# Kernel tuning notes

Hardware: AMD Instinct MI355X
Metric: run time of the kernel (lower is better)

Reference implementation:

```python
import jax, jax.numpy as jnp
import numpy as np

# Fixed architecture constants from Cifar10Model / RetNetConfig
NL = 8            # num_layers
H = 4             # num_heads
D = 64            # hidden_size
QK = 64           # qk_dim
V = 128           # v_dim
QH, VH = QK // H, V // H   # 16, 32 per-head dims
P, IMG, C = 8, 32, 3       # patch size, image size, channels
NP = (IMG // P) ** 2       # 16 patches
T = NP + 1                 # +1 cls token -> 17 tokens
FFN = 12                   # ffn_proj_size


def layer_norm(x, s, b, eps=1e-5):
    mu = x.mean(-1, keepdims=True)
    var = x.var(-1, keepdims=True)
    return (x - mu) * jax.lax.rsqrt(var + eps) * s + b


def rotate_every_two(x):
    x1, x2 = x[..., ::2], x[..., 1::2]
    return jnp.stack([-x2, x1], axis=-1).reshape(x.shape)


def rel_pos(t):
    # xPos-style rotation angles over the per-head qk dim
    angle = 1.0 / (10000 ** jnp.linspace(0.0, 1.0, QH // 2))
    angle = jnp.repeat(angle, 2)                      # (QH,)
    idx = jnp.arange(t, dtype=jnp.float32)[:, None]
    sin, cos = jnp.sin(idx * angle), jnp.cos(idx * angle)   # (t, QH)
    # per-head retention decay gamma (use_default_gamma=False path)
    gamma = 1.0 - jnp.exp(jnp.linspace(np.log(1 / 32), np.log(1 / 512), H))  # (H,)
    n = jnp.arange(t)
    expo = n[:, None] - n[None, :]                    # n - m
    causal = expo >= 0
    dmask = jnp.where(causal, gamma[:, None, None] ** jnp.where(causal, expo, 0), 0.0)  # (H,t,t)
    dmask = dmask / jnp.sqrt(dmask.sum(-1, keepdims=True))   # row-normalized decay
    return sin, cos, dmask


def retention(x, Wq, Wk, Wv, Wg, Wo, sin, cos, dmask):
    b, t, _ = x.shape
    q = (x @ Wq).reshape(b, t, H, QH).transpose(0, 2, 1, 3)   # (b,h,t,qh)
    k = (x @ Wk).reshape(b, t, H, QH).transpose(0, 2, 1, 3)
    v = (x @ Wv).reshape(b, t, H, VH).transpose(0, 2, 1, 3)   # (b,h,t,vh)
    g = x @ Wg                                                # (b,t,V) gate
    q = q * cos + rotate_every_two(q) * sin
    k = (k * cos + rotate_every_two(k) * sin) * (QH ** -0.5)
    scores = jnp.einsum('bhnd,bhmd->bhnm', q, k) * dmask      # decay-masked QK^T
    denom = jnp.clip(jnp.abs(jax.lax.stop_gradient(scores).sum(-1, keepdims=True)), 1.0, None)
    scores = scores / denom                                   # retention row normalization
    o = jnp.einsum('bhnm,bhmd->bhnd', scores, v)              # (b,h,t,vh)
    # per-head group norm (no affine) instead of softmax normalization
    mu = o.mean(-1, keepdims=True)
    var = o.var(-1, keepdims=True)
    o = (o - mu) * jax.lax.rsqrt(var + 1e-5)
    o = o.transpose(0, 2, 1, 3).reshape(b, t, V)
    return (jax.nn.silu(g) * o) @ Wo


def setup_inputs() -> dict:
    key = jax.random.key(0)
    ks = iter(jax.random.split(key, 32))
    s = 0.02
    B = 8192
    inp = {
        'x': jax.random.normal(next(ks), (B, C, IMG, IMG), jnp.float32),
        'patch_w': jax.random.normal(next(ks), (C * P * P, D), jnp.float32) * s,
        'patch_b': jnp.zeros((D,), jnp.float32),
        'cls': jax.random.normal(next(ks), (1, 1, D), jnp.float32) * s,
        'pos': jax.random.normal(next(ks), (T, D), jnp.float32) * s,
        'Wq': jax.random.normal(next(ks), (NL, D, QK), jnp.float32) * s,
        'Wk': jax.random.normal(next(ks), (NL, D, QK), jnp.float32) * s,
        'Wv': jax.random.normal(next(ks), (NL, D, V), jnp.float32) * s,
        'Wg': jax.random.normal(next(ks), (NL, D, V), jnp.float32) * s,
        'Wo': jax.random.normal(next(ks), (NL, V, D), jnp.float32) * s,
        'ln1_s': jnp.ones((NL, D), jnp.float32),
        'ln1_b': jnp.zeros((NL, D), jnp.float32),
        'w1': jax.random.normal(next(ks), (NL, D, FFN), jnp.float32) * s,
        'b1': jnp.zeros((NL, FFN), jnp.float32),
        'w2': jax.random.normal(next(ks), (NL, FFN, D), jnp.float32) * s,
        'b2': jnp.zeros((NL, D), jnp.float32),
        'ln2_s': jnp.ones((NL, D), jnp.float32),
        'ln2_b': jnp.zeros((NL, D), jnp.float32),
        'lnf_s': jnp.ones((D,), jnp.float32),
        'lnf_b': jnp.zeros((D,), jnp.float32),
        'neck_w': jax.random.normal(next(ks), (D, 16), jnp.float32) * s,
        'neck_b': jnp.zeros((16,), jnp.float32),
        'head_w': jax.random.normal(next(ks), (16, 10), jnp.float32) * s,
        'head_b': jnp.zeros((10,), jnp.float32),
    }
    return inp


def reference(x, patch_w, patch_b, cls, pos, Wq, Wk, Wv, Wg, Wo, ln1_s, ln1_b,
              w1, b1, w2, b2, ln2_s, ln2_b, lnf_s, lnf_b, neck_w, neck_b, head_w, head_b):
    b = x.shape[0]
    # patch embedding: stride==kernel conv expressed as reshape + matmul
    xp = x.reshape(b, C, IMG // P, P, IMG // P, P).transpose(0, 2, 4, 1, 3, 5)
    xp = xp.reshape(b, NP, C * P * P)
    tok = xp @ patch_w + patch_b                          # (b,16,64)
    tok = jnp.concatenate([jnp.broadcast_to(cls, (b, 1, D)), tok], axis=1) + pos  # (b,17,64)
    sin, cos, dmask = rel_pos(T)
    h = tok
    for i in range(NL):  # pre-LN RetNet blocks
        h = h + retention(layer_norm(h, ln1_s[i], ln1_b[i]),
                          Wq[i], Wk[i], Wv[i], Wg[i], Wo[i], sin, cos, dmask)
        f = layer_norm(h, ln2_s[i], ln2_b[i])
        h = h + jax.nn.gelu(f @ w1[i] + b1[i]) @ w2[i] + b2[i]
    h = layer_norm(h, lnf_s, lnf_b)
    ys = h[:, -1, :]                                      # last token
    return (ys @ neck_w + neck_b) @ head_w + head_b       # (b,10) logits
```

## Files before the change

### kernel.cpp

```cpp
#include <hip/hip_runtime.h>
#include <hip/hip_bf16.h>

#define NLAY 8
#define MFMA __builtin_amdgcn_mfma_f32_16x16x32_bf16
#define MFMA32 __builtin_amdgcn_mfma_f32_32x32x16_bf16

typedef __attribute__((ext_vector_type(8))) short bf16x8;
typedef __attribute__((ext_vector_type(4))) float f32x4;
typedef __attribute__((ext_vector_type(16))) float f32x16;
typedef __attribute__((ext_vector_type(4))) int i32x4;

template <bool BF16>
__device__ __forceinline__ float ld(const void* p, int i) {
  if (BF16) {
    unsigned short u = ((const unsigned short*)p)[i];
    return __uint_as_float(((unsigned)u) << 16);
  }
  return ((const float*)p)[i];
}

template <bool BF16>
__device__ __forceinline__ float2 ld2(const void* p, int i) {
  float2 r;
  if (BF16) {
    unsigned u = ((const unsigned*)p)[i >> 1];
    r.x = __uint_as_float(u << 16);
    r.y = __uint_as_float(u & 0xffff0000u);
  } else {
    r = ((const float2*)p)[i >> 1];
  }
  return r;
}

__device__ __forceinline__ unsigned pack_bf2(float a, float b) {
  __hip_bfloat16 ha = __float2bfloat16(a), hb = __float2bfloat16(b);
  unsigned short ua, ub;
  __builtin_memcpy(&ua, &ha, 2);
  __builtin_memcpy(&ub, &hb, 2);
  return ((unsigned)ub << 16) | (unsigned)ua;
}

__device__ __forceinline__ unsigned short cvt_bf(float a) {
  __hip_bfloat16 h = __float2bfloat16(a);
  unsigned short us;
  __builtin_memcpy(&us, &h, 2);
  return us;
}

__device__ __forceinline__ float2 unpk(unsigned u) {
  float2 r;
  r.x = __uint_as_float(u << 16);
  r.y = __uint_as_float(u & 0xffff0000u);
  return r;
}

__device__ __forceinline__ bf16x8 as_bf(i32x4 v) {
  bf16x8 r;
  __builtin_memcpy(&r, &v, 16);
  return r;
}

__global__ void setup_tables(float* __restrict__ ws, const void* __restrict__ x) {
  int tid = threadIdx.x;
  for (int idx = tid; idx < 272; idx += 256) {
    int t = idx >> 4, j = idx & 15;
    float a = powf(10000.f, -(float)(j >> 1) / 7.f);
    float arg = (float)t * a;
    ws[idx] = sinf(arg);
    ws[272 + idx] = cosf(arg);
  }
  for (int row = tid; row < 68; row += 256) {
    int hh = row / 17, t = row % 17;
    float gamma = 1.f - exp2f(-5.f - 4.f * (float)hh / 3.f);
    float sum = 0.f;
    for (int u = 0; u <= t; ++u) sum += powf(gamma, (float)(t - u));
    float rn = rsqrtf(sum);
    for (int u = 0; u < 17; ++u)
      ws[544 + row * 17 + u] = (u <= t) ? powf(gamma, (float)(t - u)) * rn : 0.f;
  }
  if (tid == 0) {
    const unsigned short* u16 = (const unsigned short*)x;
    int sane = 0;
    for (int i = 0; i < 128; ++i) {
      float v = __uint_as_float(((unsigned)u16[2 * i]) << 16);
      float av = fabsf(v);
      if (v == 0.f || (av > 1e-8f && av < 1e4f)) sane++;
    }
    ws[1700] = (sane >= 64) ? 1.f : 0.f;
  }
}

#define FRAG_OLD 280576
#define FRAG_TOT 305152
template <bool BF16>
__global__ void prep_frags(const void* __restrict__ patch_w,
                           const void* __restrict__ Wq, const void* __restrict__ Wk,
                           const void* __restrict__ Wv, const void* __restrict__ Wg,
                           const void* __restrict__ Wo, const void* __restrict__ w1,
                           const void* __restrict__ w2,
                           const float* __restrict__ tab,
                           unsigned short* __restrict__ frag) {
  if ((tab[1700] > 0.5f) != BF16) return;
  int g = blockIdx.x * 256 + threadIdx.x;
  if (g >= FRAG_TOT) return;
  float v;
  if (g < 12288) {
    int nt = g / 3072, r = g % 3072, kt = r / 512, r2 = r % 512, la = r2 >> 3, j = r2 & 7;
    int n = nt * 16 + (la & 15), k = kt * 32 + (la >> 4) * 8 + j;
    v = ld<BF16>(patch_w, k * 64 + n);
  } else if (g < FRAG_OLD) {
    int gg = g - 12288, l = gg / 33536, o = gg % 33536;
    if (o < 8192) {
      const void* W = (o < 4096) ? Wq : Wk;
      int e = o & 4095;
      int nt = e / 1024, r = e % 1024, kt = r / 512, r2 = r % 512, la = r2 >> 3, j = r2 & 7;
      int n = nt * 16 + (la & 15), k = kt * 32 + (la >> 4) * 8 + j;
      v = ld<BF16>(W, l * 4096 + k * 64 + n);
    } else if (o < 24576) {
      const void* W = (o < 16384) ? Wv : Wg;
      int e = (o - 8192) & 8191;
      int nt = e / 1024, r = e % 1024, kt = r / 512, r2 = r % 512, la = r2 >> 3, j = r2 & 7;
      int n = nt * 16 + (la & 15), k = kt * 32 + (la >> 4) * 8 + j;
      v = ld<BF16>(W, l * 8192 + k * 128 + n);
    } else if (o < 32768) {
      int e = o - 24576;
      int nt = e / 2048, r = e % 2048, kt = r / 512, r2 = r % 512, la = r2 >> 3, j = r2 & 7;
      int n = nt * 16 + (la & 15), k = kt * 32 + (la >> 4) * 8 + j;
      v = ld<BF16>(Wo, l * 8192 + k * 64 + n);
    } else {
      int e = o - 32768, eo = e / 64, d = e % 64;
      v = ld<BF16>(w1, l * 768 + d * 12 + eo);
    }
  } else {
    int gg = g - FRAG_OLD, l = gg / 3072, o = gg % 3072;
    if (o < 1024) {
      int kt = o >> 9, r = o & 511, la = r >> 3, j = r & 7;
      int n = la & 15, k = kt * 32 + (la >> 4) * 8 + j;
      v = (n < 12) ? ld<BF16>(w1, l * 768 + k * 12 + n) : 0.f;
    } else {
      int e2 = o - 1024;
      int nt = e2 >> 9, r = e2 & 511, la = r >> 3, j = r & 7;
      int n = nt * 16 + (la & 15), k = (la >> 4) * 8 + j;
      v = (k < 12) ? ld<BF16>(w2, (l * 12 + k) * 64 + n) : 0.f;
    }
  }
  __hip_bfloat16 h = __float2bfloat16(v);
  unsigned short us;
  __builtin_memcpy(&us, &h, 2);
  frag[g] = us;
}

#define O_DM   0
#define O_SIN  1156
#define O_COS  1428
#define O_ST   1700
#define O_H    2212
#define O_XNF  4456
#define O_FF   5992
#define O_R    6400
#define O_SCA  11024
#define O_VG   14096
#define SM_TOT 18968

template <bool BF16>
__global__ void __launch_bounds__(512, 4)
vit_fused(const void* __restrict__ x, const void* __restrict__ patch_b,
          const void* __restrict__ cls, const void* __restrict__ pos,
          const void* __restrict__ ln1s, const void* __restrict__ ln1b,
          const void* __restrict__ b1, const void* __restrict__ b2,
          const void* __restrict__ ln2s, const void* __restrict__ ln2b,
          const void* __restrict__ lnfs, const void* __restrict__ lnfb,
          const void* __restrict__ neckw, const void* __restrict__ neckb,
          const void* __restrict__ headw, const void* __restrict__ headb,
          const float* __restrict__ tab, const unsigned short* __restrict__ FR,
          void* __restrict__ out) {
  if ((tab[1700] > 0.5f) != BF16) return;

  const int tid = threadIdx.x;
  const int lane = tid & 63, w = tid >> 6;
  const int lq = lane >> 4, ln = lane & 15;
  const int img0 = 2 * blockIdx.x;

  __shared__ __align__(16) float sm[SM_TOT];
  float* sDM  = sm + O_DM;
  float* sSin = sm + O_SIN;
  float* sCos = sm + O_COS;
  float* sST  = sm + O_ST;
  float* sH   = sm + O_H;
  float* sFF  = sm + O_FF;
  float* sQ   = sm + O_R;
  float* sK   = sm + O_R + 2312;
  float* sO   = sm + O_R;
  unsigned short* sVbT = (unsigned short*)(sm + O_VG);
  unsigned short* sGb  = (unsigned short*)(sm + O_VG) + 5120;
  const bf16x8* FRB = (const bf16x8*)FR;

  for (int i = tid; i < 1156; i += 512) sDM[i] = tab[544 + i] * 0.25f;
  for (int i = tid; i < 272; i += 512) { sSin[i] = tab[i]; sCos[i] = tab[272 + i]; }
  for (int s = tid; s < 768; s += 512) {
    int mt = s / 384, r = s % 384, kt = r / 64, la = r % 64;
    int p = la & 15, q = la >> 4;
    int kb = kt * 32 + q * 8;
    int c = kb >> 6, rem = kb & 63, a = rem >> 3;
    int pi = p >> 2, pj = p & 3;
    int src = (img0 + mt) * 3072 + c * 1024 + (pi * 8 + a) * 32 + pj * 8;
    float v[8];
#pragma unroll
    for (int t2 = 0; t2 < 8; t2 += 2) {
      float2 pv = ld2<BF16>(x, src + t2);
      v[t2] = pv.x; v[t2 + 1] = pv.y;
    }
    i32x4 pk;
    pk.x = pack_bf2(v[0], v[1]); pk.y = pack_bf2(v[2], v[3]);
    pk.z = pack_bf2(v[4], v[5]); pk.w = pack_bf2(v[6], v[7]);
    ((i32x4*)(sm + O_SCA))[s] = pk;
  }
  if (tid < 128) {
    int img = tid >> 6, n = tid & 63;
    sH[(img * 17) * 66 + n] = ld<BF16>(cls, n) + ld<BF16>(pos, n);
  }
  __syncthreads();

  {
    int mt = w >> 2, nt = w & 3;
    f32x4 acc = {0.f, 0.f, 0.f, 0.f};
    const bf16x8* paf = (const bf16x8*)(sm + O_SCA);
#pragma unroll
    for (int kt = 0; kt < 6; ++kt)
      acc = MFMA(paf[(mt * 6 + kt) * 64 + lane], FRB[(nt * 6 + kt) * 64 + lane], acc, 0, 0, 0);
    int n = nt * 16 + ln;
    float pb = ld<BF16>(patch_b, n);
#pragma unroll
    for (int i = 0; i < 4; ++i) {
      int t = 1 + lq * 4 + i;
      sH[(mt * 17 + t) * 66 + n] = acc[i] + pb + ld<BF16>(pos, t * 64 + n);
    }
  }
  __syncthreads();

  for (int l = 0; l < NLAY; ++l) {
    const int LB = 1536 + l * 4192;

    if (tid < 320) {
      int la = tid & 63, wv = tid >> 6;
      int m = wv * 8 + (la & 7);
      int sub = ((la >> 3) & 3) + 4 * (la >> 5);
      i32x4 pk = {0, 0, 0, 0};
      if (m < 34) {
        const float2* hp = (const float2*)(sH + m * 66 + sub * 8);
        float2 h0 = hp[0], h1 = hp[1], h2 = hp[2], h3 = hp[3];
        float s1 = 0.f, s2 = 0.f;
        s1 += h0.x; s2 += h0.x * h0.x; s1 += h0.y; s2 += h0.y * h0.y;
        s1 += h1.x; s2 += h1.x * h1.x; s1 += h1.y; s2 += h1.y * h1.y;
        s1 += h2.x; s2 += h2.x * h2.x; s1 += h2.y; s2 += h2.y * h2.y;
        s1 += h3.x; s2 += h3.x * h3.x; s1 += h3.y; s2 += h3.y * h3.y;
        s1 += __shfl_xor(s1, 8);  s2 += __shfl_xor(s2, 8);
        s1 += __shfl_xor(s1, 16); s2 += __shfl_xor(s2, 16);
        s1 += __shfl_xor(s1, 32); s2 += __shfl_xor(s2, 32);
        float mu = s1 * (1.f / 64.f);
        float var = s2 * (1.f / 64.f) - mu * mu;
        float rr = rsqrtf(var + 1e-5f);
        int kb = sub * 8;
        float hv[8] = {h0.x, h0.y, h1.x, h1.y, h2.x, h2.y, h3.x, h3.y};
        float vv[8];
#pragma unroll
        for (int t2 = 0; t2 < 8; t2 += 2) {
          float2 sv = ld2<BF16>(ln1s, l * 64 + kb + t2);
          float2 bv = ld2<BF16>(ln1b, l * 64 + kb + t2);
          vv[t2]     = (hv[t2] - mu) * rr * sv.x + bv.x;
          vv[t2 + 1] = (hv[t2 + 1] - mu) * rr * sv.y + bv.y;
        }
        pk.x = pack_bf2(vv[0], vv[1]); pk.y = pack_bf2(vv[2], vv[3]);
        pk.z = pack_bf2(vv[4], vv[5]); pk.w = pack_bf2(vv[6], vv[7]);
      }
      int slot = (m >> 4) * 128 + (sub >> 2) * 64 + (sub & 3) * 16 + (m & 15);
      ((i32x4*)(sm + O_XNF))[slot] = pk;
    }
    __syncthreads();

    {
      const bf16x8* xnf = (const bf16x8*)(sm + O_XNF);
      {
        const bf16x8* wf = FRB + LB + ((w < 4) ? 0 : 512);
        float* dst = (w < 4) ? sQ : sK;
        int ntl = w & 3;
        int n = ntl * 16 + ln;
#pragma unroll
        for (int mt = 0; mt < 3; ++mt) {
          f32x4 acc = {0.f, 0.f, 0.f, 0.f};
          acc = MFMA(xnf[(mt * 2) * 64 + lane], wf[(ntl * 2) * 64 + lane], acc, 0, 0, 0);
          acc = MFMA(xnf[(mt * 2 + 1) * 64 + lane], wf[(ntl * 2 + 1) * 64 + lane], acc, 0, 0, 0);
          if (mt < 2) {
            float* p = dst + (mt * 16 + lq * 4) * 68 + n;
            p[0] = acc[0]; p[68] = acc[1]; p[136] = acc[2]; p[204] = acc[3];
          } else if (lq == 0) {
            float* p = dst + 32 * 68 + n;
            p[0] = acc[0]; p[68] = acc[1];
          }
        }
      }
      {
        const bf16x8* wf = FRB + LB + 1024;
        int n = w * 16 + ln;
#pragma unroll
        for (int mt = 0; mt < 3; ++mt) {
          f32x4 acc = {0.f, 0.f, 0.f, 0.f};
          acc = MFMA(xnf[(mt * 2) * 64 + lane], wf[(w * 2) * 64 + lane], acc, 0, 0, 0);
          acc = MFMA(xnf[(mt * 2 + 1) * 64 + lane], wf[(w * 2 + 1) * 64 + lane], acc, 0, 0, 0);
          if (mt == 0) {
            uint2 uv;
            uv.x = pack_bf2(acc[0], acc[1]);
            uv.y = pack_bf2(acc[2], acc[3]);
            *(uint2*)(sVbT + n * 20 + lq * 4) = uv;
          } else if (mt == 1) {
#pragma unroll
            for (int i = 0; i < 4; ++i) {
              int m = 16 + lq * 4 + i;
              int img = (m >= 17), t = m - img * 17;
              sVbT[img * 2560 + n * 20 + t] = cvt_bf(acc[i]);
            }
          } else if (lq == 0) {
            sVbT[2560 + n * 20 + 15] = cvt_bf(acc[0]);
            sVbT[2560 + n * 20 + 16] = cvt_bf(acc[1]);
          }
        }
      }
      {
        const bf16x8* wf = FRB + LB + 2048;
        int n = w * 16 + ln;
#pragma unroll
        for (int mt = 0; mt < 3; ++mt) {
          f32x4 acc = {0.f, 0.f, 0.f, 0.f};
          acc = MFMA(xnf[(mt * 2) * 64 + lane], wf[(w * 2) * 64 + lane], acc, 0, 0, 0);
          acc = MFMA(xnf[(mt * 2 + 1) * 64 + lane], wf[(w * 2 + 1) * 64 + lane], acc, 0, 0, 0);
          if (mt < 2) {
            unsigned short* p = sGb + (mt * 16 + lq * 4) * 136 + n;
            p[0] = cvt_bf(acc[0]); p[136] = cvt_bf(acc[1]);
            p[272] = cvt_bf(acc[2]); p[408] = cvt_bf(acc[3]);
          } else if (lq == 0) {
            sGb[32 * 136 + n] = cvt_bf(acc[0]);
            sGb[33 * 136 + n] = cvt_bf(acc[1]);
          }
        }
      }
    }
    __syncthreads();

    {
      int img = w >> 2, hh = w & 3;
      int cl = lane & 31, kh = lane >> 5;
      int tt = (cl < 17) ? cl : 16;
      int rb = (img * 17 + tt) * 68 + hh * 16 + kh * 8;
      int sb = tt * 16 + kh * 8;
      float4 s0 = *(const float4*)(sSin + sb), s1 = *(const float4*)(sSin + sb + 4);
      float4 c0 = *(const float4*)(sCos + sb), c1 = *(const float4*)(sCos + sb + 4);
      float4 qa = *(const float4*)(sQ + rb), qb = *(const float4*)(sQ + rb + 4);
      i32x4 ap;
      ap.x = pack_bf2(qa.x * c0.x - qa.y * s0.x, qa.y * c0.y + qa.x * s0.y);
      ap.y = pack_bf2(qa.z * c0.z - qa.w * s0.z, qa.w * c0.w + qa.z * s0.w);
      ap.z = pack_bf2(qb.x * c1.x - qb.y * s1.x, qb.y * c1.y + qb.x * s1.y);
      ap.w = pack_bf2(qb.z * c1.z - qb.w * s1.z, qb.w * c1.w + qb.z * s1.w);
      float4 ka = *(const float4*)(sK + rb), kb = *(const float4*)(sK + rb + 4);
      i32x4 bp;
      bp.x = pack_bf2(ka.x * c0.x - ka.y * s0.x, ka.y * c0.y + ka.x * s0.y);
      bp.y = pack_bf2(ka.z * c0.z - ka.w * s0.z, ka.w * c0.w + ka.z * s0.w);
      bp.z = pack_bf2(kb.x * c1.x - kb.y * s1.x, kb.y * c1.y + kb.x * s1.y);
      bp.w = pack_bf2(kb.z * c1.z - kb.w * s1.z, kb.w * c1.w + kb.z * s1.w);
      const unsigned short* vcol = sVbT + img * 2560 + (hh * 32 + cl) * 20 + kh * 8;
      uint2 v0 = ((const uint2*)vcol)[0], v1 = ((const uint2*)vcol)[1];
      i32x4 bpv; bpv.x = (int)v0.x; bpv.y = (int)v0.y; bpv.z = (int)v1.x; bpv.w = (int)v1.y;
      unsigned short v16 = sVbT[img * 2560 + (hh * 32 + cl) * 20 + 16];
      __syncthreads();

      f32x16 acc = {0.f, 0.f, 0.f, 0.f, 0.f, 0.f, 0.f, 0.f,
                    0.f, 0.f, 0.f, 0.f, 0.f, 0.f, 0.f, 0.f};
      acc = MFMA32(as_bf(bp), as_bf(ap), acc, 0, 0, 0);
      const float* dmr = sDM + hh * 289 + tt * 17;
      float p[16];
#pragma unroll
      for (int r = 0; r < 16; ++r) {
        int u = (r & 3) + 8 * (r >> 2) + 4 * kh;
        p[r] = (u <= 16) ? acc[r] * dmr[u] : 0.f;
      }
      float own = 0.f;
#pragma unroll
      for (int r = 0; r < 16; ++r) own += p[r];
      float den = fabsf(own + __shfl_xor(own, 32));
      if (den < 1.f) den = 1.f;
      den = 1.f / den;
      float ex[4];
#pragma unroll
      for (int j = 0; j < 4; ++j)
        ex[j] = __shfl_xor((kh == 0) ? p[4 + j] : p[j], 32);
      float pd[8];
#pragma unroll
      for (int j = 0; j < 4; ++j) {
        pd[j]     = ((kh == 0) ? p[j]  : ex[j])     * den;
        pd[4 + j] = ((kh == 0) ? ex[j] : p[4 + j])  * den;
      }
      i32x4 apv;
      apv.x = pack_bf2(pd[0], pd[1]); apv.y = pack_bf2(pd[2], pd[3]);
      apv.z = pack_bf2(pd[4], pd[5]); apv.w = pack_bf2(pd[6], pd[7]);
      f32x16 ao = {0.f, 0.f, 0.f, 0.f, 0.f, 0.f, 0.f, 0.f,
                   0.f, 0.f, 0.f, 0.f, 0.f, 0.f, 0.f, 0.f};
      ao = MFMA32(as_bf(apv), as_bf(bpv), ao, 0, 0, 0);
      i32x4 a1 = {0, 0, 0, 0}, b1v = {0, 0, 0, 0};
      if (kh == 0) {
        a1.x = (int)(unsigned)cvt_bf(p[8] * den);
        b1v.x = (int)(unsigned)v16;
      }
      ao = MFMA32(as_bf(a1), as_bf(b1v), ao, 0, 0, 0);
      int cg = hh * 32 + cl;
#pragma unroll
      for (int r = 0; r < 16; ++r) {
        int t = (r & 3) + 8 * (r >> 2) + 4 * kh;
        if (t < 17) sO[(img * 17 + t) * 134 + cg] = ao[r];
      }
    }
    __syncthreads();

    for (int s = tid; s < 768; s += 512) {
      int mt = s >> 8, kt = (s >> 6) & 3, la = s & 63;
      int q = la >> 4, m = mt * 16 + (la & 15);
      int cb = kt * 32 + q * 8;
      i32x4 pk = {0, 0, 0, 0};
      if (m < 34) {
        const float2* op = (const float2*)(sO + m * 134 + cb);
        float2 o0 = op[0], o1 = op[1], o2 = op[2], o3 = op[3];
        float s1 = 0.f, s2 = 0.f;
        s1 += o0.x; s2 += o0.x * o0.x; s1 += o0.y; s2 += o0.y * o0.y;
        s1 += o1.x; s2 += o1.x * o1.x; s1 += o1.y; s2 += o1.y * o1.y;
        s1 += o2.x; s2 += o2.x * o2.x; s1 += o2.y; s2 += o2.y * o2.y;
        s1 += o3.x; s2 += o3.x * o3.x; s1 += o3.y; s2 += o3.y * o3.y;
        s1 += __shfl_xor(s1, 16); s2 += __shfl_xor(s2, 16);
        s1 += __shfl_xor(s1, 32); s2 += __shfl_xor(s2, 32);
        float mu = s1 * (1.f / 32.f);
        float var = s2 * (1.f / 32.f) - mu * mu;
        float rr = rsqrtf(var + 1e-5f);
        i32x4 gu = *(const i32x4*)(sGb + m * 136 + cb);
        float ov[8] = {o0.x, o0.y, o1.x, o1.y, o2.x, o2.y, o3.x, o3.y};
        float vv[8];
#pragma unroll
        for (int q2 = 0; q2 < 4; ++q2) {
          unsigned gw = (q2 == 0) ? (unsigned)gu.x : (q2 == 1) ? (unsigned)gu.y
                       : (q2 == 2) ? (unsigned)gu.z : (unsigned)gu.w;
          float2 gv = unpk(gw);
          float on0 = (ov[2 * q2] - mu) * rr;
          float on1 = (ov[2 * q2 + 1] - mu) * rr;
          vv[2 * q2]     = on0 * (gv.x / (1.f + __expf(-gv.x)));
          vv[2 * q2 + 1] = on1 * (gv.y / (1.f + __expf(-gv.y)));
        }
        pk.x = pack_bf2(vv[0], vv[1]); pk.y = pack_bf2(vv[2], vv[3]);
        pk.z = pack_bf2(vv[4], vv[5]); pk.w = pack_bf2(vv[6], vv[7]);
      }
      ((i32x4*)(sm + O_SCA))[s] = pk;
    }
    __syncthreads();

    {
      const bf16x8* oaf = (const bf16x8*)(sm + O_SCA);
      const bf16x8* wof = FRB + LB + 3072;
      for (int j = w; j < 12; j += 8) {
        int mt = j >> 2, nt = j & 3;
        f32x4 acc = {0.f, 0.f, 0.f, 0.f};
#pragma unroll
        for (int kt = 0; kt < 4; ++kt)
          acc = MFMA(oaf[(mt * 4 + kt) * 64 + lane], wof[(nt * 4 + kt) * 64 + lane], acc, 0, 0, 0);
        int n = nt * 16 + ln;
#pragma unroll
        for (int i = 0; i < 4; ++i) {
          int m = mt * 16 + lq * 4 + i;
          if (m < 34) sH[m * 66 + n] += acc[i];
        }
      }
    }
    __syncthreads();

    if (tid < 320) {
      int la = tid & 63, wv = tid >> 6;
      int m = wv * 8 + (la & 7);
      int sub = ((la >> 3) & 3) + 4 * (la >> 5);
      i32x4 pk = {0, 0, 0, 0};
      if (m < 34) {
        const float2* hp = (const float2*)(sH + m * 66 + sub * 8);
        float2 h0 = hp[0], h1 = hp[1], h2 = hp[2], h3 = hp[3];
        float s1 = 0.f, s2 = 0.f;
        s1 += h0.x; s2 += h0.x * h0.x; s1 += h0.y; s2 += h0.y * h0.y;
        s1 += h1.x; s2 += h1.x * h1.x; s1 += h1.y; s2 += h1.y * h1.y;
        s1 += h2.x; s2 += h2.x * h2.x; s1 += h2.y; s2 += h2.y * h2.y;
        s1 += h3.x; s2 += h3.x * h3.x; s1 += h3.y; s2 += h3.y * h3.y;
        s1 += __shfl_xor(s1, 8);  s2 += __shfl_xor(s2, 8);
        s1 += __shfl_xor(s1, 16); s2 += __shfl_xor(s2, 16);
        s1 += __shfl_xor(s1, 32); s2 += __shfl_xor(s2, 32);
        float mu = s1 * (1.f / 64.f);
        float var = s2 * (1.f / 64.f) - mu * mu;
        float rr = rsqrtf(var + 1e-5f);
        int kb = sub * 8;
        float hv[8] = {h0.x, h0.y, h1.x, h1.y, h2.x, h2.y, h3.x, h3.y};
        float vv[8];
#pragma unroll
        for (int t2 = 0; t2 < 8; t2 += 2) {
          float2 sv = ld2<BF16>(ln2s, l * 64 + kb + t2);
          float2 bv = ld2<BF16>(ln2b, l * 64 + kb + t2);
          vv[t2]     = (hv[t2] - mu) * rr * sv.x + bv.x;
          vv[t2 + 1] = (hv[t2 + 1] - mu) * rr * sv.y + bv.y;
        }
        pk.x = pack_bf2(vv[0], vv[1]); pk.y = pack_bf2(vv[2], vv[3]);
        pk.z = pack_bf2(vv[4], vv[5]); pk.w = pack_bf2(vv[6], vv[7]);
      }
      int slot = (m >> 4) * 128 + (sub >> 2) * 64 + (sub & 3) * 16 + (m & 15);
      ((i32x4*)(sm + O_XNF))[slot] = pk;
    }
    __syncthreads();

    if (w < 3) {
      const bf16x8* xnf = (const bf16x8*)(sm + O_XNF);
      const bf16x8* w1f = FRB + 35072 + l * 384;
      int mt = w;
      f32x4 acc = {0.f, 0.f, 0.f, 0.f};
#pragma unroll
      for (int kt = 0; kt < 2; ++kt)
        acc = MFMA(xnf[(mt * 2 + kt) * 64 + lane], w1f[kt * 64 + lane], acc, 0, 0, 0);
      if (ln < 12) {
        float b = ld<BF16>(b1, l * 12 + ln);
#pragma unroll
        for (int i = 0; i < 4; ++i) {
          int m = mt * 16 + lq * 4 + i;
          if (m < 34) {
            float a = acc[i] + b;
            float inner = 0.7978845608028654f * (a + 0.044715f * a * a * a);
            float e = __expf(2.f * inner);
            float th = 1.f - 2.f / (e + 1.f);
            sFF[m * 12 + ln] = 0.5f * a * (1.f + th);
          }
        }
      }
    }
    __syncthreads();

    {
      const bf16x8* w2f = FRB + 35072 + l * 384 + 128;
      for (int j = w; j < 12; j += 8) {
        int mt = j >> 2, nt = j & 3;
        i32x4 ap = {0, 0, 0, 0};
        int ma = mt * 16 + ln;
        if (ma < 34) {
          const float* fp = sFF + ma * 12;
          if (lq == 0) {
            ap.x = pack_bf2(fp[0], fp[1]); ap.y = pack_bf2(fp[2], fp[3]);
            ap.z = pack_bf2(fp[4], fp[5]); ap.w = pack_bf2(fp[6], fp[7]);
          } else if (lq == 1) {
            ap.x = pack_bf2(fp[8], fp[9]); ap.y = pack_bf2(fp[10], fp[11]);
          }
        }
        f32x4 acc = {0.f, 0.f, 0.f, 0.f};
        acc = MFMA(as_bf(ap), w2f[nt * 64 + lane], acc, 0, 0, 0);
        int n = nt * 16 + ln;
        float b = ld<BF16>(b2, l * 64 + n);
#pragma unroll
        for (int i = 0; i < 4; ++i) {
          int m = mt * 16 + lq * 4 + i;
          if (m < 34) sH[m * 66 + n] += acc[i] + b;
        }
      }
    }
    __syncthreads();
  }

  if (tid < 2) {
    int m = tid * 17 + 16;
    float s1 = 0.f, s2 = 0.f;
    for (int d = 0; d < 64; ++d) {
      float v = sH[m * 66 + d];
      s1 += v; s2 += v * v;
    }
    float mu = s1 * (1.f / 64.f);
    float var = s2 * (1.f / 64.f) - mu * mu;
    sST[tid] = mu;
    sST[2 + tid] = rsqrtf(var + 1e-5f);
  }
  __syncthreads();
  if (tid < 32) {
    int img = tid >> 4, jn = tid & 15;
    int m = img * 17 + 16;
    float mu = sST[img], rr = sST[2 + img];
    float acc = ld<BF16>(neckb, jn);
    for (int d = 0; d < 64; ++d) {
      float yn = (sH[m * 66 + d] - mu) * rr * ld<BF16>(lnfs, d) + ld<BF16>(lnfb, d);
      acc += yn * ld<BF16>(neckw, d * 16 + jn);
    }
    sST[8 + img * 16 + jn] = acc;
  }
  __syncthreads();
  if (tid < 20) {
    int img = tid / 10, o = tid % 10;
    float acc = ld<BF16>(headb, o);
#pragma unroll
    for (int e = 0; e < 16; ++e) acc += sST[8 + img * 16 + e] * ld<BF16>(headw, e * 10 + o);
    if (BF16) {
      ((__hip_bfloat16*)out)[(img0 + img) * 10 + o] = __float2bfloat16(acc);
    } else {
      ((float*)out)[(img0 + img) * 10 + o] = acc;
    }
  }
}

extern "C" void kernel_launch(void* const* d_in, const int* in_sizes, int n_in,
                              void* d_out, int out_size, void* d_ws, size_t ws_size,
                              hipStream_t stream) {
  float* tab = (float*)d_ws;
  unsigned short* frag = (unsigned short*)((char*)d_ws + 8192);

  setup_tables<<<dim3(1), dim3(256), 0, stream>>>(tab, d_in[0]);

  const int prepBlocks = (FRAG_TOT + 255) / 256;
  prep_frags<false><<<dim3(prepBlocks), dim3(256), 0, stream>>>(
      d_in[1], d_in[5], d_in[6], d_in[7], d_in[8], d_in[9], d_in[12], d_in[14], tab, frag);
  prep_frags<true><<<dim3(prepBlocks), dim3(256), 0, stream>>>(
      d_in[1], d_in[5], d_in[6], d_in[7], d_in[8], d_in[9], d_in[12], d_in[14], tab, frag);

  const int B = in_sizes[0] / 3072;
  const int grid = B / 2;

  vit_fused<false><<<dim3(grid), dim3(512), 0, stream>>>(
      d_in[0], d_in[2], d_in[3], d_in[4], d_in[10], d_in[11], d_in[13],
      d_in[15], d_in[16], d_in[17], d_in[18], d_in[19], d_in[20], d_in[21],
      d_in[22], d_in[23], tab, frag, d_out);
  vit_fused<true><<<dim3(grid), dim3(512), 0, stream>>>(
      d_in[0], d_in[2], d_in[3], d_in[4], d_in[10], d_in[11], d_in[13],
      d_in[15], d_in[16], d_in[17], d_in[18], d_in[19], d_in[20], d_in[21],
      d_in[22], d_in[23], tab, frag, d_out);
}
```

Measured before the change: 762.7 us.

## Fuse rotary embedding into Q/K projection epilogue and store bf16 Q/K

```diff
diff --git a/kernel.cpp b/kernel.cpp
--- a/kernel.cpp
+++ b/kernel.cpp
@@ -58,6 +58,22 @@
   bf16x8 r;
   __builtin_memcpy(&r, &v, 16);
   return r;
+}
+
+template <bool BF16>
+__device__ __forceinline__ void ld8v(const void* p, int i, float* v) {
+  if (BF16) {
+    i32x4 u = *(const i32x4*)((const unsigned short*)p + i);
+    float2 a = unpk((unsigned)u.x); v[0] = a.x; v[1] = a.y;
+    float2 b = unpk((unsigned)u.y); v[2] = b.x; v[3] = b.y;
+    float2 c = unpk((unsigned)u.z); v[4] = c.x; v[5] = c.y;
+    float2 d = unpk((unsigned)u.w); v[6] = d.x; v[7] = d.y;
+  } else {
+    float4 a = *(const float4*)((const float*)p + i);
+    float4 b = *(const float4*)((const float*)p + i + 4);
+    v[0] = a.x; v[1] = a.y; v[2] = a.z; v[3] = a.w;
+    v[4] = b.x; v[5] = b.y; v[6] = b.z; v[7] = b.w;
+  }
 }
 
 __global__ void setup_tables(float* __restrict__ ws, const void* __restrict__ x) {
@@ -188,8 +204,8 @@
   float* sST  = sm + O_ST;
   float* sH   = sm + O_H;
   float* sFF  = sm + O_FF;
-  float* sQ   = sm + O_R;
-  float* sK   = sm + O_R + 2312;
+  unsigned short* sQb = (unsigned short*)(sm + O_R);
+  unsigned short* sKb = ((unsigned short*)(sm + O_R)) + 2312;
   float* sO   = sm + O_R;
   unsigned short* sVbT = (unsigned short*)(sm + O_VG);
   unsigned short* sGb  = (unsigned short*)(sm + O_VG) + 5120;
@@ -262,14 +278,13 @@
         float rr = rsqrtf(var + 1e-5f);
         int kb = sub * 8;
         float hv[8] = {h0.x, h0.y, h1.x, h1.y, h2.x, h2.y, h3.x, h3.y};
+        float sv[8], bv[8];
+        ld8v<BF16>(ln1s, l * 64 + kb, sv);
+        ld8v<BF16>(ln1b, l * 64 + kb, bv);
         float vv[8];
 #pragma unroll
-        for (int t2 = 0; t2 < 8; t2 += 2) {
-          float2 sv = ld2<BF16>(ln1s, l * 64 + kb + t2);
-          float2 bv = ld2<BF16>(ln1b, l * 64 + kb + t2);
-          vv[t2]     = (hv[t2] - mu) * rr * sv.x + bv.x;
-          vv[t2 + 1] = (hv[t2 + 1] - mu) * rr * sv.y + bv.y;
-        }
+        for (int t2 = 0; t2 < 8; ++t2)
+          vv[t2] = (hv[t2] - mu) * rr * sv[t2] + bv[t2];
         pk.x = pack_bf2(vv[0], vv[1]); pk.y = pack_bf2(vv[2], vv[3]);
         pk.z = pack_bf2(vv[4], vv[5]); pk.w = pack_bf2(vv[6], vv[7]);
       }
@@ -282,20 +297,31 @@
       const bf16x8* xnf = (const bf16x8*)(sm + O_XNF);
       {
         const bf16x8* wf = FRB + LB + ((w < 4) ? 0 : 512);
-        float* dst = (w < 4) ? sQ : sK;
+        unsigned short* dst = (w < 4) ? sQb : sKb;
         int ntl = w & 3;
         int n = ntl * 16 + ln;
+        int j0 = n & 14;
+        float sgn = (n & 1) ? 1.f : -1.f;
 #pragma unroll
         for (int mt = 0; mt < 3; ++mt) {
           f32x4 acc = {0.f, 0.f, 0.f, 0.f};
           acc = MFMA(xnf[(mt * 2) * 64 + lane], wf[(ntl * 2) * 64 + lane], acc, 0, 0, 0);
           acc = MFMA(xnf[(mt * 2 + 1) * 64 + lane], wf[(ntl * 2 + 1) * 64 + lane], acc, 0, 0, 0);
+          unsigned short rbf[4];
+#pragma unroll
+          for (int i = 0; i < 4; ++i) {
+            float part = __shfl_xor(acc[i], 1);
+            int t = lq * 4 + i - mt;
+            if (t < 0) t += 17;
+            float cv = sCos[t * 16 + j0], sv = sSin[t * 16 + j0];
+            rbf[i] = cvt_bf(acc[i] * cv + part * (sgn * sv));
+          }
           if (mt < 2) {
-            float* p = dst + (mt * 16 + lq * 4) * 68 + n;
-            p[0] = acc[0]; p[68] = acc[1]; p[136] = acc[2]; p[204] = acc[3];
+            unsigned short* p = dst + (mt * 16 + lq * 4) * 68 + n;
+            p[0] = rbf[0]; p[68] = rbf[1]; p[136] = rbf[2]; p[204] = rbf[3];
           } else if (lq == 0) {
-            float* p = dst + 32 * 68 + n;
-            p[0] = acc[0]; p[68] = acc[1];
+            unsigned short* p = dst + 32 * 68 + n;
+            p[0] = rbf[0]; p[68] = rbf[1];
           }
         }
       }
@@ -350,22 +376,14 @@
       int img = w >> 2, hh = w & 3;
       int cl = lane & 31, kh = lane >> 5;
       int tt = (cl < 17) ? cl : 16;
-      int rb = (img * 17 + tt) * 68 + hh * 16 + kh * 8;
-      int sb = tt * 16 + kh * 8;
-      float4 s0 = *(const float4*)(sSin + sb), s1 = *(const float4*)(sSin + sb + 4);
-      float4 c0 = *(const float4*)(sCos + sb), c1 = *(const float4*)(sCos + sb + 4);
-      float4 qa = *(const float4*)(sQ + rb), qb = *(const float4*)(sQ + rb + 4);
-      i32x4 ap;
-      ap.x = pack_bf2(qa.x * c0.x - qa.y * s0.x, qa.y * c0.y + qa.x * s0.y);
-      ap.y = pack_bf2(qa.z * c0.z - qa.w * s0.z, qa.w * c0.w + qa.z * s0.w);
-      ap.z = pack_bf2(qb.x * c1.x - qb.y * s1.x, qb.y * c1.y + qb.x * s1.y);
-      ap.w = pack_bf2(qb.z * c1.z - qb.w * s1.z, qb.w * c1.w + qb.z * s1.w);
-      float4 ka = *(const float4*)(sK + rb), kb = *(const float4*)(sK + rb + 4);
-      i32x4 bp;
-      bp.x = pack_bf2(ka.x * c0.x - ka.y * s0.x, ka.y * c0.y + ka.x * s0.y);
-      bp.y = pack_bf2(ka.z * c0.z - ka.w * s0.z, ka.w * c0.w + ka.z * s0.w);
-      bp.z = pack_bf2(kb.x * c1.x - kb.y * s1.x, kb.y * c1.y + kb.x * s1.y);
-      bp.w = pack_bf2(kb.z * c1.z - kb.w * s1.z, kb.w * c1.w + kb.z * s1.w);
+      int m = img * 17 + tt;
+      int off = m * 68 + hh * 16 + kh * 8;
+      const uint2* qr = (const uint2*)(sQb + off);
+      uint2 q0 = qr[0], q1 = qr[1];
+      const uint2* kr = (const uint2*)(sKb + off);
+      uint2 k0 = kr[0], k1 = kr[1];
+      i32x4 ap; ap.x = (int)q0.x; ap.y = (int)q0.y; ap.z = (int)q1.x; ap.w = (int)q1.y;
+      i32x4 bp; bp.x = (int)k0.x; bp.y = (int)k0.y; bp.z = (int)k1.x; bp.w = (int)k1.y;
       const unsigned short* vcol = sVbT + img * 2560 + (hh * 32 + cl) * 20 + kh * 8;
       uint2 v0 = ((const uint2*)vcol)[0], v1 = ((const uint2*)vcol)[1];
       i32x4 bpv; bpv.x = (int)v0.x; bpv.y = (int)v0.y; bpv.z = (int)v1.x; bpv.w = (int)v1.y;
@@ -387,7 +405,7 @@
       for (int r = 0; r < 16; ++r) own += p[r];
       float den = fabsf(own + __shfl_xor(own, 32));
       if (den < 1.f) den = 1.f;
-      den = 1.f / den;
+      den = __builtin_amdgcn_rcpf(den);
       float ex[4];
 #pragma unroll
       for (int j = 0; j < 4; ++j)
@@ -447,8 +465,8 @@
           float2 gv = unpk(gw);
           float on0 = (ov[2 * q2] - mu) * rr;
           float on1 = (ov[2 * q2 + 1] - mu) * rr;
-          vv[2 * q2]     = on0 * (gv.x / (1.f + __expf(-gv.x)));
-          vv[2 * q2 + 1] = on1 * (gv.y / (1.f + __expf(-gv.y)));
+          vv[2 * q2]     = on0 * gv.x * __builtin_amdgcn_rcpf(1.f + __expf(-gv.x));
+          vv[2 * q2 + 1] = on1 * gv.y * __builtin_amdgcn_rcpf(1.f + __expf(-gv.y));
         }
         pk.x = pack_bf2(vv[0], vv[1]); pk.y = pack_bf2(vv[2], vv[3]);
         pk.z = pack_bf2(vv[4], vv[5]); pk.w = pack_bf2(vv[6], vv[7]);
@@ -497,14 +515,13 @@
         float rr = rsqrtf(var + 1e-5f);
         int kb = sub * 8;
         float hv[8] = {h0.x, h0.y, h1.x, h1.y, h2.x, h2.y, h3.x, h3.y};
+        float sv[8], bv[8];
+        ld8v<BF16>(ln2s, l * 64 + kb, sv);
+        ld8v<BF16>(ln2b, l * 64 + kb, bv);
         float vv[8];
 #pragma unroll
-        for (int t2 = 0; t2 < 8; t2 += 2) {
-          float2 sv = ld2<BF16>(ln2s, l * 64 + kb + t2);
-          float2 bv = ld2<BF16>(ln2b, l * 64 + kb + t2);
-          vv[t2]     = (hv[t2] - mu) * rr * sv.x + bv.x;
-          vv[t2 + 1] = (hv[t2 + 1] - mu) * rr * sv.y + bv.y;
-        }
+        for (int t2 = 0; t2 < 8; ++t2)
+          vv[t2] = (hv[t2] - mu) * rr * sv[t2] + bv[t2];
         pk.x = pack_bf2(vv[0], vv[1]); pk.y = pack_bf2(vv[2], vv[3]);
         pk.z = pack_bf2(vv[4], vv[5]); pk.w = pack_bf2(vv[6], vv[7]);
       }
@@ -530,7 +547,7 @@
             float a = acc[i] + b;
             float inner = 0.7978845608028654f * (a + 0.044715f * a * a * a);
             float e = __expf(2.f * inner);
-            float th = 1.f - 2.f / (e + 1.f);
+            float th = 1.f - 2.f * __builtin_amdgcn_rcpf(e + 1.f);
             sFF[m * 12 + ln] = 0.5f * a * (1.f + th);
           }
         }
@@ -545,12 +562,14 @@
         i32x4 ap = {0, 0, 0, 0};
         int ma = mt * 16 + ln;
         if (ma < 34) {
-          const float* fp = sFF + ma * 12;
+          const float4* fp4 = (const float4*)(sFF + ma * 12);
           if (lq == 0) {
-            ap.x = pack_bf2(fp[0], fp[1]); ap.y = pack_bf2(fp[2], fp[3]);
-            ap.z = pack_bf2(fp[4], fp[5]); ap.w = pack_bf2(fp[6], fp[7]);
+            float4 a = fp4[0], b4 = fp4[1];
+            ap.x = pack_bf2(a.x, a.y); ap.y = pack_bf2(a.z, a.w);
+            ap.z = pack_bf2(b4.x, b4.y); ap.w = pack_bf2(b4.z, b4.w);
           } else if (lq == 1) {
-            ap.x = pack_bf2(fp[8], fp[9]); ap.y = pack_bf2(fp[10], fp[11]);
+            float4 c4 = fp4[2];
+            ap.x = pack_bf2(c4.x, c4.y); ap.y = pack_bf2(c4.z, c4.w);
           }
         }
         f32x4 acc = {0.f, 0.f, 0.f, 0.f};
```

Result: faster. 727.3 us (-4.6%).
